# Kernel tuning notes

Measured on AMD Instinct MI355X. Metric: run time of the kernel, lower is better.

Reference implementation:

```python
import jax, jax.numpy as jnp
import numpy as np

DIM = 1024
NUM_HEADS = 16
HEAD_DIM = DIM // NUM_HEADS
WINDOW = 1024
GATE_IN = 20
B, T = 2, 2048
ROPE_BASE = 10000.0


def setup_inputs() -> dict:
    key = jax.random.key(0)
    ks = jax.random.split(key, 12)
    s = 0.02
    x = jax.random.normal(ks[0], (B, T, DIM), dtype=jnp.float32)
    Wq = jax.random.normal(ks[1], (DIM, DIM), dtype=jnp.float32) * s
    bq = jnp.zeros((DIM,), jnp.float32)
    Wk = jax.random.normal(ks[2], (DIM, DIM), dtype=jnp.float32) * s
    bk = jnp.zeros((DIM,), jnp.float32)
    Wv = jax.random.normal(ks[3], (DIM, DIM), dtype=jnp.float32) * s
    bv = jnp.zeros((DIM,), jnp.float32)
    # o_lin.weight is zero-initialized in the original; use random here so the
    # reference output/grads are non-degenerate.
    Wo = jax.random.normal(ks[4], (DIM, DIM), dtype=jnp.float32) * s
    bo = jnp.zeros((DIM,), jnp.float32)
    Wg = jax.random.normal(ks[5], (NUM_HEADS, GATE_IN), dtype=jnp.float32) * s
    bg = jnp.zeros((NUM_HEADS,), jnp.float32)
    # rotary tables, half-dim convention
    inv_freq = 1.0 / (ROPE_BASE ** (jnp.arange(0, HEAD_DIM, 2, dtype=jnp.float32) / HEAD_DIM))
    t = jnp.arange(T, dtype=jnp.float32)
    freqs = jnp.outer(t, inv_freq)  # [T, HEAD_DIM/2]
    return {"x": x, "Wq": Wq, "bq": bq, "Wk": Wk, "bk": bk, "Wv": Wv, "bv": bv,
            "Wo": Wo, "bo": bo, "Wg": Wg, "bg": bg,
            "cos": jnp.cos(freqs), "sin": jnp.sin(freqs)}


def _rope(u, cos, sin):
    # u: [B,T,H,hd]; cos/sin: [T, hd/2]
    u1, u2 = jnp.split(u, 2, axis=-1)
    c = cos[None, :, None, :]
    s = sin[None, :, None, :]
    return jnp.concatenate([u1 * c - u2 * s, u1 * s + u2 * c], axis=-1)


def reference(x, Wq, bq, Wk, bk, Wv, bv, Wo, bo, Wg, bg, cos, sin):
    Bx, Tx, D = x.shape
    q = (x @ Wq.T + bq).reshape(Bx, Tx, NUM_HEADS, HEAD_DIM)
    k = (x @ Wk.T + bk).reshape(Bx, Tx, NUM_HEADS, HEAD_DIM)
    v = (x @ Wv.T + bv).reshape(Bx, Tx, NUM_HEADS, HEAD_DIM)
    q = _rope(q, cos, sin)
    k = _rope(k, cos, sin)
    scale = 1.0 / jnp.sqrt(jnp.float32(HEAD_DIM))
    scores = jnp.einsum('bqhd,bkhd->bhqk', q, k) * scale  # [B,H,T,T]
    i = jnp.arange(Tx)[:, None]
    j = jnp.arange(Tx)[None, :]
    mask = (j <= i) & (j >= i - WINDOW)  # causal + sliding window (WINDOW left, 0 right)
    scores = jnp.where(mask[None, None], scores, jnp.float32(-1e30))
    probs = jax.nn.softmax(scores, axis=-1)
    o = jnp.einsum('bhqk,bkhd->bqhd', probs, v)  # [B,T,H,hd]
    gate = jax.nn.sigmoid(x[..., :GATE_IN] @ Wg.T + bg)  # [B,T,H]
    o = o * gate[..., None]
    o = o.reshape(Bx, Tx, D)
    return o @ Wo.T + bo
```

## Files before the change

### kernel.cpp

```cpp
#include <hip/hip_runtime.h>

#define DIMM 1024
#define NHEADS 16
#define HDIM 64
#define WIN 1024
#define GATEIN 20
#define BB 2
#define TT 2048
#define MTOT (BB*TT)

typedef __attribute__((ext_vector_type(8))) short short8;
typedef __attribute__((ext_vector_type(4))) float f32x4;
typedef __attribute__((ext_vector_type(16))) float f32x16;
typedef const __attribute__((address_space(1))) void gvoid_t;
typedef __attribute__((address_space(3))) void lvoid_t;

__device__ __forceinline__ unsigned short f2b(float f) {
  union { float f; unsigned u; } c; c.f = f;
  unsigned u = c.u + 0x7fffu + ((c.u >> 16) & 1u);
  return (unsigned short)(u >> 16);
}
__device__ __forceinline__ float b2f(unsigned short s) {
  union { unsigned u; float f; } c; c.u = ((unsigned)s) << 16;
  return c.f;
}
__device__ __forceinline__ unsigned cvt_pk_bf16(float lo, float hi) {
  unsigned r;
  asm("v_cvt_pk_bf16_f32 %0, %1, %2" : "=v"(r) : "v"(lo), "v"(hi));
  return r;
}
__device__ __forceinline__ float xmax32(float x) {
  union { float f; unsigned u; } c; c.f = x;
  auto pr = __builtin_amdgcn_permlane32_swap(c.u, c.u, false, false);
  union { unsigned u; float f; } a, b; a.u = pr[0]; b.u = pr[1];
  return fmaxf(a.f, b.f);
}
__device__ __forceinline__ float xsum32(float x) {
  union { float f; unsigned u; } c; c.f = x;
  auto pr = __builtin_amdgcn_permlane32_swap(c.u, c.u, false, false);
  union { unsigned u; float f; } a, b; a.u = pr[0]; b.u = pr[1];
  return a.f + b.f;
}

__global__ void prep_kernel(const float* __restrict__ x,  const float* __restrict__ Wq,
                            const float* __restrict__ Wk, const float* __restrict__ Wv,
                            const float* __restrict__ Wo, const float* __restrict__ bq,
                            const float* __restrict__ bk, const float* __restrict__ bv,
                            unsigned short* __restrict__ xb, unsigned short* __restrict__ wqkv,
                            unsigned short* __restrict__ wob, float* __restrict__ bcat) {
  int i = blockIdx.x * blockDim.x + threadIdx.x;
  const float* src; unsigned short* dst; int off;
  if (i < 1048576)      { src = x;  dst = xb;             off = i; }
  else if (i < 1310720) { src = Wq; dst = wqkv;           off = i - 1048576; }
  else if (i < 1572864) { src = Wk; dst = wqkv + 1048576; off = i - 1310720; }
  else if (i < 1835008) { src = Wv; dst = wqkv + 2097152; off = i - 1572864; }
  else if (i < 2097152) { src = Wo; dst = wob;            off = i - 1835008; }
  else {
    int j = i - 2097152;
    if (j < 768) {
      const float* bsrc = (j < 256) ? bq : (j < 512) ? bk : bv;
      int bo = (j & 255) * 4;
      int db = (j < 256) ? 0 : (j < 512) ? 1024 : 2048;
      *(float4*)(bcat + db + bo) = *(const float4*)(bsrc + bo);
    }
    return;
  }
  float4 v = ((const float4*)src)[off];
  union { unsigned short s[4]; uint2 u; } o;
  o.s[0] = f2b(v.x); o.s[1] = f2b(v.y); o.s[2] = f2b(v.z); o.s[3] = f2b(v.w);
  *(uint2*)(dst + (size_t)off * 4) = o.u;
}

__global__ void gate_kernel(const float* __restrict__ x, const float* __restrict__ Wg,
                            const float* __restrict__ bg, float* __restrict__ gate) {
  int i = blockIdx.x * blockDim.x + threadIdx.x;
  if (i >= MTOT * NHEADS) return;
  int h = i & 15;
  int m = i >> 4;
  const float* xr = x + (size_t)m * DIMM;
  const float* wr = Wg + h * GATEIN;
  float z = bg[h];
#pragma unroll
  for (int g = 0; g < GATEIN; ++g) z += xr[g] * wr[g];
  gate[i] = 1.f / (1.f + __expf(-z));
}

template<int MF, int OUTBF>
__global__ __launch_bounds__(256) void gemm_bt(const unsigned short* __restrict__ A,
                                               const unsigned short* __restrict__ Bw,
                                               const float* __restrict__ bias,
                                               void* __restrict__ Cout,
                                               int M, int N, int K) {
  __shared__ __align__(16) unsigned short As[MF * 32 * 32];
  __shared__ __align__(16) unsigned short Bs[128 * 32];
  const int tid = threadIdx.x;
  const int lane = tid & 63, wid = tid >> 6;
  const int g = lane >> 4, r16 = lane & 15;
  const int m0 = blockIdx.y * (MF * 32), n0 = blockIdx.x * 128;
  const int wr = (wid >> 1) * (MF * 16), wc = (wid & 1) * 64;
  const int wbase = wid * 64;

  const unsigned short* paf[MF];
  const unsigned short* pbf[4];
#pragma unroll
  for (int mf = 0; mf < MF; ++mf) {
    int row = wr + mf * 16 + r16;
    paf[mf] = As + row * 32 + ((g ^ ((row >> 1) & 3)) * 8);
  }
#pragma unroll
  for (int nf = 0; nf < 4; ++nf) {
    int row = wc + nf * 16 + r16;
    pbf[nf] = Bs + row * 32 + ((g ^ ((row >> 1) & 3)) * 8);
  }

  f32x4 acc[MF][4];
#pragma unroll
  for (int i = 0; i < MF; ++i)
#pragma unroll
    for (int j = 0; j < 4; ++j) acc[i][j] = (f32x4){0.f, 0.f, 0.f, 0.f};

  for (int k0 = 0; k0 < K; k0 += 32) {
#pragma unroll
    for (int j = 0; j < MF / 2; ++j) {
      int sbase = j * 256 + wbase;
      int s = sbase + lane;
      int l = s ^ ((s >> 3) & 3);
      const unsigned short* gA = A + (size_t)(m0 + (l >> 2)) * K + k0 + (l & 3) * 8;
      __builtin_amdgcn_global_load_lds((gvoid_t*)gA, (lvoid_t*)((char*)As + sbase * 16), 16, 0, 0);
    }
#pragma unroll
    for (int j = 0; j < 2; ++j) {
      int sbase = j * 256 + wbase;
      int s = sbase + lane;
      int l = s ^ ((s >> 3) & 3);
      const unsigned short* gB = Bw + (size_t)(n0 + (l >> 2)) * K + k0 + (l & 3) * 8;
      __builtin_amdgcn_global_load_lds((gvoid_t*)gB, (lvoid_t*)((char*)Bs + sbase * 16), 16, 0, 0);
    }
    __syncthreads();
    short8 af[MF], bf[4];
#pragma unroll
    for (int mf = 0; mf < MF; ++mf) af[mf] = *(const short8*)(paf[mf]);
#pragma unroll
    for (int nf = 0; nf < 4; ++nf)  bf[nf] = *(const short8*)(pbf[nf]);
#pragma unroll
    for (int mf = 0; mf < MF; ++mf)
#pragma unroll
      for (int nf = 0; nf < 4; ++nf)
        acc[mf][nf] = __builtin_amdgcn_mfma_f32_16x16x32_bf16(af[mf], bf[nf], acc[mf][nf], 0, 0, 0);
    __syncthreads();
  }
#pragma unroll
  for (int mf = 0; mf < MF; ++mf)
#pragma unroll
    for (int nf = 0; nf < 4; ++nf)
#pragma unroll
      for (int rr = 0; rr < 4; ++rr) {
        int m = m0 + wr + mf * 16 + g * 4 + rr;
        int n = n0 + wc + nf * 16 + r16;
        float v = acc[mf][nf][rr] + bias[n];
        if (OUTBF) ((unsigned short*)Cout)[(size_t)m * N + n] = f2b(v);
        else       ((float*)Cout)[(size_t)m * N + n] = v;
      }
}

#define QSCALE (0.125f * 1.4426950408889634f)
__global__ void rope_kernel(const unsigned short* __restrict__ qkv,
                            const float* __restrict__ cosb, const float* __restrict__ sinb,
                            unsigned short* __restrict__ qr, unsigned short* __restrict__ kr) {
  int i = blockIdx.x * blockDim.x + threadIdx.x;
  if (i >= MTOT * NHEADS * 32) return;
  int d = i & 31;
  int h = (i >> 5) & 15;
  int m = i >> 9;
  int t = m & (TT - 1);
  int b = m >> 11;
  const unsigned short* row = qkv + (size_t)m * 3072;
  float c = cosb[t * 32 + d], s = sinb[t * 32 + d];
  float q1 = b2f(row[h * 64 + d]),        q2 = b2f(row[h * 64 + d + 32]);
  float k1 = b2f(row[1024 + h * 64 + d]), k2 = b2f(row[1024 + h * 64 + d + 32]);
  size_t base = (size_t)(b * NHEADS + h) * TT * HDIM;
  size_t oq = base + (size_t)t * HDIM + d;
  qr[oq]      = f2b((q1 * c - q2 * s) * QSCALE);
  qr[oq + 32] = f2b((q1 * s + q2 * c) * QSCALE);
  size_t ok = base + (size_t)(t >> 5) * 2048 + (size_t)(d >> 4) * 512
            + (size_t)((d >> 3) & 1) * 256 + (size_t)(t & 31) * 8 + (d & 7);
  kr[ok]        = f2b(k1 * c - k2 * s);
  kr[ok + 1024] = f2b(k1 * s + k2 * c);
}

__global__ __launch_bounds__(256) void vtrans_kernel(const unsigned short* __restrict__ qkv,
                                                     unsigned short* __restrict__ vt) {
  __shared__ unsigned short tile[64][66];
  const int t0 = blockIdx.x * 64;
  const int bh = blockIdx.y;
  const int b = bh >> 4, h = bh & 15;
  const int tid = threadIdx.x;
  const int r = tid >> 2;
  const int c0 = (tid & 3) * 16;
  {
    const unsigned short* src = qkv + (size_t)(b * TT + t0 + r) * 3072 + 2048 + h * 64 + c0;
    short8 v0 = *(const short8*)src;
    short8 v1 = *(const short8*)(src + 8);
#pragma unroll
    for (int j = 0; j < 8; ++j) {
      tile[r][c0 + j] = (unsigned short)v0[j];
      tile[r][c0 + 8 + j] = (unsigned short)v1[j];
    }
  }
  __syncthreads();
  {
    const int d = tid >> 2;
    const int tc = (tid & 3) * 16;
    short8 o0, o1;
#pragma unroll
    for (int j = 0; j < 8; ++j) {
      o0[j] = (short)tile[tc + j][d];
      o1[j] = (short)tile[tc + 8 + j][d];
    }
    int kt = (t0 + tc) >> 5;
    int n  = (tc >> 4) & 1;
    int m  = d >> 5, l31v = d & 31;
    size_t A0 = (size_t)bh * TT * HDIM + (size_t)kt * 2048
              + (size_t)(m * 2 + n) * 512 + (size_t)l31v * 8;
    *(short8*)(vt + A0)       = o0;
    *(short8*)(vt + A0 + 256) = o1;
  }
}

__global__ __launch_bounds__(256) void attn_kernel(const unsigned short* __restrict__ qr,
                                                   const unsigned short* __restrict__ kr,
                                                   const unsigned short* __restrict__ vt,
                                                   const float* __restrict__ gate,
                                                   unsigned short* __restrict__ attn_out) {
  __shared__ float lds_m[4][32];
  __shared__ float lds_l[4][32];
  __shared__ float lds_O[3][64][33];
  const int tid = threadIdx.x;
  const int lane = tid & 63, wid = tid >> 6;
  const int l31 = lane & 31, hi = lane >> 5;

  const int fid = blockIdx.x;
  const int idx = fid >> 3;
  const int bh = (fid & 7) * 4 + (idx & 3);
  const int qt = 63 - (idx >> 2);
  const int q0 = qt * 32;
  const int b = bh >> 4, h = bh & 15;
  const unsigned short* kptr = kr + (size_t)bh * TT * HDIM;
  const unsigned short* vptr = vt + (size_t)bh * TT * HDIM;
  const int q = q0 + l31;

  short8 qf[4];
#pragma unroll
  for (int st = 0; st < 4; ++st)
    qf[st] = *(const short8*)(qr + (size_t)bh * TT * HDIM + (size_t)q * HDIM + st * 16 + hi * 8);

  f32x16 o0, o1;
#pragma unroll
  for (int r = 0; r < 16; ++r) { o0[r] = 0.f; o1[r] = 0.f; }
  float mrun = -1e30f, lrun = 0.f;

  int kv_lo = q0 - WIN;
  if (kv_lo < 0) kv_lo = 0;
  const int kv_hi = q0 + 32;

  for (int kv = kv_lo + wid * 32; kv < kv_hi; kv += 128) {
    const unsigned short* kf = kptr + (size_t)kv * 64 + lane * 8;
    short8 k0 = *(const short8*)(kf);
    short8 k1 = *(const short8*)(kf + 512);
    short8 k2 = *(const short8*)(kf + 1024);
    short8 k3 = *(const short8*)(kf + 1536);
    const unsigned short* vf = vptr + (size_t)kv * 64 + lane * 8;
    short8 vf00 = *(const short8*)(vf);
    short8 vf01 = *(const short8*)(vf + 512);
    short8 vf10 = *(const short8*)(vf + 1024);
    short8 vf11 = *(const short8*)(vf + 1536);

    f32x16 s;
#pragma unroll
    for (int r = 0; r < 16; ++r) s[r] = 0.f;
    s = __builtin_amdgcn_mfma_f32_32x32x16_bf16(k0, qf[0], s, 0, 0, 0);
    s = __builtin_amdgcn_mfma_f32_32x32x16_bf16(k1, qf[1], s, 0, 0, 0);
    s = __builtin_amdgcn_mfma_f32_32x32x16_bf16(k2, qf[2], s, 0, 0, 0);
    s = __builtin_amdgcn_mfma_f32_32x32x16_bf16(k3, qf[3], s, 0, 0, 0);

    float sv[16];
    if (kv == q0) {
#pragma unroll
      for (int r = 0; r < 16; ++r) {
        int key = kv + (r & 3) + 8 * (r >> 2) + 4 * hi;
        sv[r] = (key <= q) ? s[r] : -1e30f;
      }
    } else if (q0 >= WIN && kv == kv_lo) {
#pragma unroll
      for (int r = 0; r < 16; ++r) {
        int key = kv + (r & 3) + 8 * (r >> 2) + 4 * hi;
        sv[r] = (key + WIN >= q) ? s[r] : -1e30f;
      }
    } else {
#pragma unroll
      for (int r = 0; r < 16; ++r) sv[r] = s[r];
    }

    float a0 = fmaxf(sv[0], sv[1]),   a1 = fmaxf(sv[2], sv[3]);
    float a2 = fmaxf(sv[4], sv[5]),   a3 = fmaxf(sv[6], sv[7]);
    float a4 = fmaxf(sv[8], sv[9]),   a5 = fmaxf(sv[10], sv[11]);
    float a6 = fmaxf(sv[12], sv[13]), a7 = fmaxf(sv[14], sv[15]);
    float b0 = fmaxf(a0, a1), b1 = fmaxf(a2, a3), b2 = fmaxf(a4, a5), b3 = fmaxf(a6, a7);
    float lm = fmaxf(fmaxf(b0, b1), fmaxf(b2, b3));
    lm = xmax32(lm);

    if (!__all(lm - mrun <= 8.f)) {
      float mnew = fmaxf(mrun, lm);
      float scf = __builtin_exp2f(mrun - mnew);
      mrun = mnew;
      lrun *= scf;
#pragma unroll
      for (int r = 0; r < 16; ++r) { o0[r] *= scf; o1[r] *= scf; }
    }

    float pv[16];
#pragma unroll
    for (int r = 0; r < 16; ++r) pv[r] = __builtin_exp2f(sv[r] - mrun);
    float c0 = (pv[0] + pv[1]) + (pv[2] + pv[3]);
    float c1 = (pv[4] + pv[5]) + (pv[6] + pv[7]);
    float c2 = (pv[8] + pv[9]) + (pv[10] + pv[11]);
    float c3 = (pv[12] + pv[13]) + (pv[14] + pv[15]);
    lrun += xsum32((c0 + c1) + (c2 + c3));

    unsigned w0 = cvt_pk_bf16(pv[0],  pv[1]),  w1 = cvt_pk_bf16(pv[2],  pv[3]);
    unsigned w2 = cvt_pk_bf16(pv[4],  pv[5]),  w3 = cvt_pk_bf16(pv[6],  pv[7]);
    unsigned w4 = cvt_pk_bf16(pv[8],  pv[9]),  w5 = cvt_pk_bf16(pv[10], pv[11]);
    unsigned w6 = cvt_pk_bf16(pv[12], pv[13]), w7 = cvt_pk_bf16(pv[14], pv[15]);
    auto s1 = __builtin_amdgcn_permlane32_swap(w0, w2, false, false);
    auto s2 = __builtin_amdgcn_permlane32_swap(w1, w3, false, false);
    auto s3 = __builtin_amdgcn_permlane32_swap(w4, w6, false, false);
    auto s4 = __builtin_amdgcn_permlane32_swap(w5, w7, false, false);
    union { unsigned u[4]; short8 s8; } pf0, pf1;
    pf0.u[0] = s1[0]; pf0.u[1] = s2[0]; pf0.u[2] = s1[1]; pf0.u[3] = s2[1];
    pf1.u[0] = s3[0]; pf1.u[1] = s4[0]; pf1.u[2] = s3[1]; pf1.u[3] = s4[1];

    o0 = __builtin_amdgcn_mfma_f32_32x32x16_bf16(vf00, pf0.s8, o0, 0, 0, 0);
    o1 = __builtin_amdgcn_mfma_f32_32x32x16_bf16(vf10, pf0.s8, o1, 0, 0, 0);
    o0 = __builtin_amdgcn_mfma_f32_32x32x16_bf16(vf01, pf1.s8, o0, 0, 0, 0);
    o1 = __builtin_amdgcn_mfma_f32_32x32x16_bf16(vf11, pf1.s8, o1, 0, 0, 0);
  }

  if (hi == 0) { lds_m[wid][l31] = mrun; lds_l[wid][l31] = lrun; }
  __syncthreads();
  float m0 = lds_m[0][l31], m1 = lds_m[1][l31], m2 = lds_m[2][l31], m3 = lds_m[3][l31];
  float mstar = fmaxf(fmaxf(m0, m1), fmaxf(m2, m3));
  float myscale = __builtin_exp2f(mrun - mstar);
  if (wid != 0) {
#pragma unroll
    for (int r = 0; r < 16; ++r) {
      lds_O[wid - 1][lane][r]      = o0[r] * myscale;
      lds_O[wid - 1][lane][16 + r] = o1[r] * myscale;
    }
  }
  __syncthreads();
  if (wid == 0) {
    float lstar = __builtin_exp2f(m0 - mstar) * lds_l[0][l31]
                + __builtin_exp2f(m1 - mstar) * lds_l[1][l31]
                + __builtin_exp2f(m2 - mstar) * lds_l[2][l31]
                + __builtin_exp2f(m3 - mstar) * lds_l[3][l31];
    float gv = gate[((size_t)b * TT + q) * NHEADS + h];
    float inv = gv / lstar;
    float of0[16], of1[16];
#pragma unroll
    for (int r = 0; r < 16; ++r) {
      of0[r] = o0[r] * myscale + lds_O[0][lane][r]      + lds_O[1][lane][r]      + lds_O[2][lane][r];
      of1[r] = o1[r] * myscale + lds_O[0][lane][16 + r] + lds_O[1][lane][16 + r] + lds_O[2][lane][16 + r];
    }
    unsigned short* orow = attn_out + ((size_t)b * TT + q) * DIMM + h * HDIM;
#pragma unroll
    for (int a2 = 0; a2 < 4; ++a2) {
      int d0 = a2 * 8 + hi * 4;
      union { unsigned short s[4]; uint2 u; } x0, x1;
#pragma unroll
      for (int c = 0; c < 4; ++c) {
        x0.s[c] = f2b(of0[a2 * 4 + c] * inv);
        x1.s[c] = f2b(of1[a2 * 4 + c] * inv);
      }
      *(uint2*)(orow + d0) = x0.u;
      *(uint2*)(orow + 32 + d0) = x1.u;
    }
  }
}

#define OFF_XB    ((size_t)0)
#define OFF_WQKV  ((size_t)8388608)
#define OFF_WO    ((size_t)14680064)
#define OFF_BCAT  ((size_t)16777216)
#define OFF_QKV   ((size_t)16793600)
#define OFF_QR    ((size_t)41959424)
#define OFF_KR    ((size_t)50348032)
#define OFF_VT    ((size_t)58736640)
#define OFF_ATTN  ((size_t)67125248)
#define OFF_GATE  ((size_t)75513856)

extern "C" void kernel_launch(void* const* d_in, const int* in_sizes, int n_in,
                              void* d_out, int out_size, void* d_ws, size_t ws_size,
                              hipStream_t stream) {
  const float* x    = (const float*)d_in[0];
  const float* Wq   = (const float*)d_in[1];
  const float* bq   = (const float*)d_in[2];
  const float* Wk   = (const float*)d_in[3];
  const float* bk   = (const float*)d_in[4];
  const float* Wv   = (const float*)d_in[5];
  const float* bv   = (const float*)d_in[6];
  const float* Wo   = (const float*)d_in[7];
  const float* bo   = (const float*)d_in[8];
  const float* Wg   = (const float*)d_in[9];
  const float* bg   = (const float*)d_in[10];
  const float* cosb = (const float*)d_in[11];
  const float* sinb = (const float*)d_in[12];
  float* out = (float*)d_out;
  char* ws = (char*)d_ws;

  unsigned short* xb    = (unsigned short*)(ws + OFF_XB);
  unsigned short* wqkv  = (unsigned short*)(ws + OFF_WQKV);
  unsigned short* wob   = (unsigned short*)(ws + OFF_WO);
  float*          bcat  = (float*)(ws + OFF_BCAT);
  unsigned short* qkv   = (unsigned short*)(ws + OFF_QKV);
  unsigned short* q_r   = (unsigned short*)(ws + OFF_QR);
  unsigned short* k_r   = (unsigned short*)(ws + OFF_KR);
  unsigned short* v_t   = (unsigned short*)(ws + OFF_VT);
  unsigned short* attn  = (unsigned short*)(ws + OFF_ATTN);
  float*          gateb = (float*)(ws + OFF_GATE);

  prep_kernel<<<8195, 256, 0, stream>>>(x, Wq, Wk, Wv, Wo, bq, bk, bv, xb, wqkv, wob, bcat);
  gate_kernel<<<256, 256, 0, stream>>>(x, Wg, bg, gateb);

  gemm_bt<4, 1><<<dim3(24, 32), 256, 0, stream>>>(xb, wqkv, bcat, qkv, MTOT, 3072, 1024);

  rope_kernel<<<8192, 256, 0, stream>>>(qkv, cosb, sinb, q_r, k_r);
  vtrans_kernel<<<dim3(32, 32), 256, 0, stream>>>(qkv, v_t);

  attn_kernel<<<2048, 256, 0, stream>>>(q_r, k_r, v_t, gateb, attn);

  gemm_bt<2, 0><<<dim3(8, 64), 256, 0, stream>>>(attn, wob, bo, out, MTOT, 1024, 1024);
}
```

Baseline: 119.7 us.

## Fuse RoPE into V-transpose kernel and compute softmax row sums via MFMA

```diff
diff --git a/kernel.cpp b/kernel.cpp
--- a/kernel.cpp
+++ b/kernel.cpp
@@ -29,17 +29,14 @@
   asm("v_cvt_pk_bf16_f32 %0, %1, %2" : "=v"(r) : "v"(lo), "v"(hi));
   return r;
 }
+__device__ __forceinline__ float max3f(float a, float b, float c) {
+  return fmaxf(fmaxf(a, b), c);
+}
 __device__ __forceinline__ float xmax32(float x) {
   union { float f; unsigned u; } c; c.f = x;
   auto pr = __builtin_amdgcn_permlane32_swap(c.u, c.u, false, false);
   union { unsigned u; float f; } a, b; a.u = pr[0]; b.u = pr[1];
   return fmaxf(a.f, b.f);
-}
-__device__ __forceinline__ float xsum32(float x) {
-  union { float f; unsigned u; } c; c.f = x;
-  auto pr = __builtin_amdgcn_permlane32_swap(c.u, c.u, false, false);
-  union { unsigned u; float f; } a, b; a.u = pr[0]; b.u = pr[1];
-  return a.f + b.f;
 }
 
 __global__ void prep_kernel(const float* __restrict__ x,  const float* __restrict__ Wq,
@@ -164,50 +161,65 @@
 }
 
 #define QSCALE (0.125f * 1.4426950408889634f)
-__global__ void rope_kernel(const unsigned short* __restrict__ qkv,
-                            const float* __restrict__ cosb, const float* __restrict__ sinb,
-                            unsigned short* __restrict__ qr, unsigned short* __restrict__ kr) {
-  int i = blockIdx.x * blockDim.x + threadIdx.x;
-  if (i >= MTOT * NHEADS * 32) return;
-  int d = i & 31;
-  int h = (i >> 5) & 15;
-  int m = i >> 9;
-  int t = m & (TT - 1);
-  int b = m >> 11;
-  const unsigned short* row = qkv + (size_t)m * 3072;
-  float c = cosb[t * 32 + d], s = sinb[t * 32 + d];
-  float q1 = b2f(row[h * 64 + d]),        q2 = b2f(row[h * 64 + d + 32]);
-  float k1 = b2f(row[1024 + h * 64 + d]), k2 = b2f(row[1024 + h * 64 + d + 32]);
-  size_t base = (size_t)(b * NHEADS + h) * TT * HDIM;
-  size_t oq = base + (size_t)t * HDIM + d;
-  qr[oq]      = f2b((q1 * c - q2 * s) * QSCALE);
-  qr[oq + 32] = f2b((q1 * s + q2 * c) * QSCALE);
-  size_t ok = base + (size_t)(t >> 5) * 2048 + (size_t)(d >> 4) * 512
-            + (size_t)((d >> 3) & 1) * 256 + (size_t)(t & 31) * 8 + (d & 7);
-  kr[ok]        = f2b(k1 * c - k2 * s);
-  kr[ok + 1024] = f2b(k1 * s + k2 * c);
-}
-
-__global__ __launch_bounds__(256) void vtrans_kernel(const unsigned short* __restrict__ qkv,
-                                                     unsigned short* __restrict__ vt) {
+__global__ __launch_bounds__(256) void ropev_kernel(const unsigned short* __restrict__ qkv,
+                                                    const float* __restrict__ cosb,
+                                                    const float* __restrict__ sinb,
+                                                    unsigned short* __restrict__ qr,
+                                                    unsigned short* __restrict__ kr,
+                                                    unsigned short* __restrict__ vt) {
   __shared__ unsigned short tile[64][66];
   const int t0 = blockIdx.x * 64;
   const int bh = blockIdx.y;
   const int b = bh >> 4, h = bh & 15;
   const int tid = threadIdx.x;
-  const int r = tid >> 2;
-  const int c0 = (tid & 3) * 16;
+  const int tr = tid >> 2;
+  const int qd = tid & 3;
+  const int t = t0 + tr;
+  const size_t base = (size_t)bh * TT * HDIM;
+  const unsigned short* row = qkv + (size_t)(b * TT + t) * 3072 + h * 64;
+
   {
-    const unsigned short* src = qkv + (size_t)(b * TT + t0 + r) * 3072 + 2048 + h * 64 + c0;
-    short8 v0 = *(const short8*)src;
-    short8 v1 = *(const short8*)(src + 8);
+    const unsigned short* vsrc = row + 2048 + qd * 16;
+    short8 v0 = *(const short8*)vsrc;
+    short8 v1 = *(const short8*)(vsrc + 8);
 #pragma unroll
     for (int j = 0; j < 8; ++j) {
-      tile[r][c0 + j] = (unsigned short)v0[j];
-      tile[r][c0 + 8 + j] = (unsigned short)v1[j];
-    }
+      tile[tr][qd * 16 + j]     = (unsigned short)v0[j];
+      tile[tr][qd * 16 + 8 + j] = (unsigned short)v1[j];
+    }
+  }
+
+  {
+    const int d0 = qd * 8;
+    short8 q1 = *(const short8*)(row + d0);
+    short8 q2 = *(const short8*)(row + d0 + 32);
+    short8 k1 = *(const short8*)(row + 1024 + d0);
+    short8 k2 = *(const short8*)(row + 1024 + d0 + 32);
+    float4 c0 = *(const float4*)(cosb + t * 32 + d0);
+    float4 c1 = *(const float4*)(cosb + t * 32 + d0 + 4);
+    float4 s0 = *(const float4*)(sinb + t * 32 + d0);
+    float4 s1 = *(const float4*)(sinb + t * 32 + d0 + 4);
+    float cc[8] = {c0.x, c0.y, c0.z, c0.w, c1.x, c1.y, c1.z, c1.w};
+    float ss[8] = {s0.x, s0.y, s0.z, s0.w, s1.x, s1.y, s1.z, s1.w};
+    short8 qo1, qo2, ko1, ko2;
+#pragma unroll
+    for (int j = 0; j < 8; ++j) {
+      float a1 = b2f((unsigned short)q1[j]), a2 = b2f((unsigned short)q2[j]);
+      float b1 = b2f((unsigned short)k1[j]), b2v = b2f((unsigned short)k2[j]);
+      qo1[j] = (short)f2b((a1 * cc[j] - a2 * ss[j]) * QSCALE);
+      qo2[j] = (short)f2b((a1 * ss[j] + a2 * cc[j]) * QSCALE);
+      ko1[j] = (short)f2b(b1 * cc[j] - b2v * ss[j]);
+      ko2[j] = (short)f2b(b1 * ss[j] + b2v * cc[j]);
+    }
+    *(short8*)(qr + base + (size_t)t * HDIM + d0)      = qo1;
+    *(short8*)(qr + base + (size_t)t * HDIM + d0 + 32) = qo2;
+    size_t ok = base + (size_t)(t >> 5) * 2048 + (size_t)(qd >> 1) * 512
+              + (size_t)(qd & 1) * 256 + (size_t)(t & 31) * 8;
+    *(short8*)(kr + ok)        = ko1;
+    *(short8*)(kr + ok + 1024) = ko2;
   }
   __syncthreads();
+
   {
     const int d = tid >> 2;
     const int tc = (tid & 3) * 16;
@@ -220,8 +232,7 @@
     int kt = (t0 + tc) >> 5;
     int n  = (tc >> 4) & 1;
     int m  = d >> 5, l31v = d & 31;
-    size_t A0 = (size_t)bh * TT * HDIM + (size_t)kt * 2048
-              + (size_t)(m * 2 + n) * 512 + (size_t)l31v * 8;
+    size_t A0 = base + (size_t)kt * 2048 + (size_t)(m * 2 + n) * 512 + (size_t)l31v * 8;
     *(short8*)(vt + A0)       = o0;
     *(short8*)(vt + A0 + 256) = o1;
   }
@@ -254,9 +265,14 @@
   for (int st = 0; st < 4; ++st)
     qf[st] = *(const short8*)(qr + (size_t)bh * TT * HDIM + (size_t)q * HDIM + st * 16 + hi * 8);
 
-  f32x16 o0, o1;
-#pragma unroll
-  for (int r = 0; r < 16; ++r) { o0[r] = 0.f; o1[r] = 0.f; }
+  f32x16 SZERO;
+#pragma unroll
+  for (int r = 0; r < 16; ++r) SZERO[r] = 0.f;
+  short8 ONES;
+#pragma unroll
+  for (int j = 0; j < 8; ++j) ONES[j] = (short)0x3F80;
+
+  f32x16 o0 = SZERO, o1 = SZERO;
   float mrun = -1e30f, lrun = 0.f;
 
   int kv_lo = q0 - WIN;
@@ -276,37 +292,31 @@
     short8 vf11 = *(const short8*)(vf + 1536);
 
     f32x16 s;
-#pragma unroll
-    for (int r = 0; r < 16; ++r) s[r] = 0.f;
-    s = __builtin_amdgcn_mfma_f32_32x32x16_bf16(k0, qf[0], s, 0, 0, 0);
+    s = __builtin_amdgcn_mfma_f32_32x32x16_bf16(k0, qf[0], SZERO, 0, 0, 0);
     s = __builtin_amdgcn_mfma_f32_32x32x16_bf16(k1, qf[1], s, 0, 0, 0);
     s = __builtin_amdgcn_mfma_f32_32x32x16_bf16(k2, qf[2], s, 0, 0, 0);
     s = __builtin_amdgcn_mfma_f32_32x32x16_bf16(k3, qf[3], s, 0, 0, 0);
 
-    float sv[16];
     if (kv == q0) {
 #pragma unroll
       for (int r = 0; r < 16; ++r) {
         int key = kv + (r & 3) + 8 * (r >> 2) + 4 * hi;
-        sv[r] = (key <= q) ? s[r] : -1e30f;
+        s[r] = (key <= q) ? s[r] : -1e30f;
       }
     } else if (q0 >= WIN && kv == kv_lo) {
 #pragma unroll
       for (int r = 0; r < 16; ++r) {
         int key = kv + (r & 3) + 8 * (r >> 2) + 4 * hi;
-        sv[r] = (key + WIN >= q) ? s[r] : -1e30f;
+        s[r] = (key + WIN >= q) ? s[r] : -1e30f;
       }
-    } else {
-#pragma unroll
-      for (int r = 0; r < 16; ++r) sv[r] = s[r];
-    }
-
-    float a0 = fmaxf(sv[0], sv[1]),   a1 = fmaxf(sv[2], sv[3]);
-    float a2 = fmaxf(sv[4], sv[5]),   a3 = fmaxf(sv[6], sv[7]);
-    float a4 = fmaxf(sv[8], sv[9]),   a5 = fmaxf(sv[10], sv[11]);
-    float a6 = fmaxf(sv[12], sv[13]), a7 = fmaxf(sv[14], sv[15]);
-    float b0 = fmaxf(a0, a1), b1 = fmaxf(a2, a3), b2 = fmaxf(a4, a5), b3 = fmaxf(a6, a7);
-    float lm = fmaxf(fmaxf(b0, b1), fmaxf(b2, b3));
+    }
+
+    float t0 = max3f(s[0],  s[1],  s[2]);
+    float t1 = max3f(s[3],  s[4],  s[5]);
+    float t2 = max3f(s[6],  s[7],  s[8]);
+    float t3 = max3f(s[9],  s[10], s[11]);
+    float t4 = max3f(s[12], s[13], s[14]);
+    float lm = fmaxf(max3f(t0, t1, t2), max3f(t3, t4, s[15]));
     lm = xmax32(lm);
 
     if (!__all(lm - mrun <= 8.f)) {
@@ -318,31 +328,31 @@
       for (int r = 0; r < 16; ++r) { o0[r] *= scf; o1[r] *= scf; }
     }
 
-    float pv[16];
-#pragma unroll
-    for (int r = 0; r < 16; ++r) pv[r] = __builtin_exp2f(sv[r] - mrun);
-    float c0 = (pv[0] + pv[1]) + (pv[2] + pv[3]);
-    float c1 = (pv[4] + pv[5]) + (pv[6] + pv[7]);
-    float c2 = (pv[8] + pv[9]) + (pv[10] + pv[11]);
-    float c3 = (pv[12] + pv[13]) + (pv[14] + pv[15]);
-    lrun += xsum32((c0 + c1) + (c2 + c3));
-
-    unsigned w0 = cvt_pk_bf16(pv[0],  pv[1]),  w1 = cvt_pk_bf16(pv[2],  pv[3]);
-    unsigned w2 = cvt_pk_bf16(pv[4],  pv[5]),  w3 = cvt_pk_bf16(pv[6],  pv[7]);
-    unsigned w4 = cvt_pk_bf16(pv[8],  pv[9]),  w5 = cvt_pk_bf16(pv[10], pv[11]);
-    unsigned w6 = cvt_pk_bf16(pv[12], pv[13]), w7 = cvt_pk_bf16(pv[14], pv[15]);
-    auto s1 = __builtin_amdgcn_permlane32_swap(w0, w2, false, false);
-    auto s2 = __builtin_amdgcn_permlane32_swap(w1, w3, false, false);
-    auto s3 = __builtin_amdgcn_permlane32_swap(w4, w6, false, false);
-    auto s4 = __builtin_amdgcn_permlane32_swap(w5, w7, false, false);
+#pragma unroll
+    for (int r = 0; r < 16; ++r) s[r] = __builtin_exp2f(s[r] - mrun);
+
+    unsigned w0 = cvt_pk_bf16(s[0],  s[1]),  w1 = cvt_pk_bf16(s[2],  s[3]);
+    unsigned w2 = cvt_pk_bf16(s[4],  s[5]),  w3 = cvt_pk_bf16(s[6],  s[7]);
+    unsigned w4 = cvt_pk_bf16(s[8],  s[9]),  w5 = cvt_pk_bf16(s[10], s[11]);
+    unsigned w6 = cvt_pk_bf16(s[12], s[13]), w7 = cvt_pk_bf16(s[14], s[15]);
+    auto s1p = __builtin_amdgcn_permlane32_swap(w0, w2, false, false);
+    auto s2p = __builtin_amdgcn_permlane32_swap(w1, w3, false, false);
+    auto s3p = __builtin_amdgcn_permlane32_swap(w4, w6, false, false);
+    auto s4p = __builtin_amdgcn_permlane32_swap(w5, w7, false, false);
     union { unsigned u[4]; short8 s8; } pf0, pf1;
-    pf0.u[0] = s1[0]; pf0.u[1] = s2[0]; pf0.u[2] = s1[1]; pf0.u[3] = s2[1];
-    pf1.u[0] = s3[0]; pf1.u[1] = s4[0]; pf1.u[2] = s3[1]; pf1.u[3] = s4[1];
+    pf0.u[0] = s1p[0]; pf0.u[1] = s2p[0]; pf0.u[2] = s1p[1]; pf0.u[3] = s2p[1];
+    pf1.u[0] = s3p[0]; pf1.u[1] = s4p[0]; pf1.u[2] = s3p[1]; pf1.u[3] = s4p[1];
+
+    f32x16 ls;
+    ls = __builtin_amdgcn_mfma_f32_32x32x16_bf16(ONES, pf0.s8, SZERO, 0, 0, 0);
+    ls = __builtin_amdgcn_mfma_f32_32x32x16_bf16(ONES, pf1.s8, ls, 0, 0, 0);
 
     o0 = __builtin_amdgcn_mfma_f32_32x32x16_bf16(vf00, pf0.s8, o0, 0, 0, 0);
     o1 = __builtin_amdgcn_mfma_f32_32x32x16_bf16(vf10, pf0.s8, o1, 0, 0, 0);
     o0 = __builtin_amdgcn_mfma_f32_32x32x16_bf16(vf01, pf1.s8, o0, 0, 0, 0);
     o1 = __builtin_amdgcn_mfma_f32_32x32x16_bf16(vf11, pf1.s8, o1, 0, 0, 0);
+
+    lrun += ls[0];
   }
 
   if (hi == 0) { lds_m[wid][l31] = mrun; lds_l[wid][l31] = lrun; }
@@ -433,8 +443,7 @@
 
   gemm_bt<4, 1><<<dim3(24, 32), 256, 0, stream>>>(xb, wqkv, bcat, qkv, MTOT, 3072, 1024);
 
-  rope_kernel<<<8192, 256, 0, stream>>>(qkv, cosb, sinb, q_r, k_r);
-  vtrans_kernel<<<dim3(32, 32), 256, 0, stream>>>(qkv, v_t);
+  ropev_kernel<<<dim3(32, 32), 256, 0, stream>>>(qkv, cosb, sinb, q_r, k_r, v_t);
 
   attn_kernel<<<2048, 256, 0, stream>>>(q_r, k_r, v_t, gateb, attn);
 
```

Result: faster. 114.6 us (-4.3%).
